# Kernel tuning notes

Measured on AMD Instinct MI355X. Metric: run time of the kernel, lower is better.

The kernel has to match this reference:

```python
import jax, jax.numpy as jnp
import numpy as np

HIDDEN = 128
N_H = 32
E = 262144


def setup_inputs() -> dict:
    key = jax.random.key(0)
    ks = jax.random.split(key, 10)
    s = lambda fan_in: 1.0 / np.sqrt(fan_in)
    return {
        "h_i": jax.random.normal(ks[0], (E, N_H), dtype=jnp.float32),
        "e_ij": jax.random.normal(ks[1], (E, 1), dtype=jnp.float32),
        # lin_A1: 1 -> HIDDEN
        "W_A1": jax.random.uniform(ks[2], (1, HIDDEN), jnp.float32, -s(1), s(1)),
        "b_A1": jnp.zeros((HIDDEN,), jnp.float32),
        # lin_A2: HIDDEN -> N_H*N_H
        "W_A2": jax.random.uniform(ks[3], (HIDDEN, N_H * N_H), jnp.float32, -s(HIDDEN), s(HIDDEN)),
        "b_A2": jnp.zeros((N_H * N_H,), jnp.float32),
        # lin_b1: 1 -> HIDDEN
        "W_b1": jax.random.uniform(ks[4], (1, HIDDEN), jnp.float32, -s(1), s(1)),
        "b_b1": jnp.zeros((HIDDEN,), jnp.float32),
        # lin_b2: HIDDEN -> N_H
        "W_b2": jax.random.uniform(ks[5], (HIDDEN, N_H), jnp.float32, -s(HIDDEN), s(HIDDEN)),
        "b_b2": jnp.zeros((N_H,), jnp.float32),
    }


def reference(h_i, e_ij, W_A1, b_A1, W_A2, b_A2, W_b1, b_b1, W_b2, b_b2):
    # Per-edge MLP producing an [N_H, N_H] matrix A from the scalar edge feature
    A = jax.nn.selu(e_ij @ W_A1 + b_A1)          # [E, HIDDEN]
    A = (A @ W_A2 + b_A2).reshape(-1, N_H, N_H)  # [E, N_H, N_H]
    # Per-edge MLP producing an [N_H] bias b
    b = jax.nn.selu(e_ij @ W_b1 + b_b1)          # [E, HIDDEN]
    b = b @ W_b2 + b_b2                          # [E, N_H]
    # Batched matvec: m_ij[e, i] = sum_j A[e, i, j] * h_i[e, j] + b[e, i]
    m_ij = jnp.einsum('eij,ej->ei', A, h_i) + b
    return m_ij
```

## Files before the change

kernel.cpp:

```cpp
#include <hip/hip_runtime.h>

#define NH      32
#define HID     128
#define E_TOT   262144
#define P_WT    4352
#define K_EXT   4256
#define CH_S    16
#define NCHUNK  8
#define LDSW_P  520

typedef float        f32x4 __attribute__((ext_vector_type(4)));
typedef short        s16x8 __attribute__((ext_vector_type(8)));
typedef unsigned int u32x4 __attribute__((ext_vector_type(4)));

static __device__ __forceinline__ short f2bf(float f) {
    __bf16 b = (__bf16)f;
    return __builtin_bit_cast(short, b);
}
static __device__ __forceinline__ float selu_f(float x) {
    const float kScale  = 1.0507009873554804934193349852946f;
    const float kAlphaS = 1.7580993408473768599402175208123f;
    float neg = kAlphaS * (__expf(x) - 1.0f);
    return x > 0.0f ? kScale * x : neg;
}

__global__ void wt_build(const float* __restrict__ W_A2, const float* __restrict__ b_A2,
                         const float* __restrict__ W_b2, unsigned short* __restrict__ WT) {
    int gid = blockIdx.x * 256 + threadIdx.x;
    if (gid >= 32 * K_EXT) return;
    int i = gid / K_EXT;
    int kap = gid - i * K_EXT;
    float v;
    if (kap < 4096) {
        int k = kap >> 5, j = kap & 31;
        v = W_A2[k * 1024 + i * 32 + j];
    } else if (kap < 4128) {
        int j = kap - 4096;
        v = b_A2[i * 32 + j];
    } else {
        int t = kap - 4128;
        v = W_b2[t * 32 + i];
    }
    WT[i * P_WT + kap] = (unsigned short)f2bf(v);
}

typedef const __attribute__((address_space(1))) unsigned int GU32;
typedef __attribute__((address_space(3))) unsigned int LU32;
static __device__ __forceinline__ void gload_lds16(const void* g, void* l) {
    __builtin_amdgcn_global_load_lds((GU32*)g, (LU32*)l, 16, 0, 0);
}

__global__ void __launch_bounds__(256, 3)
msg_main(const float* __restrict__ h_i, const float* __restrict__ e_ij,
         const float* __restrict__ W_A1, const float* __restrict__ b_A1,
         const float* __restrict__ W_b1, const float* __restrict__ b_b1,
         const float* __restrict__ b_b2,
         const unsigned short* __restrict__ WT,
         float* __restrict__ out)
{
    __shared__ unsigned short ldsW[32 * LDSW_P];
    __shared__ float ut[CH_S][256];
    __shared__ float cA1[HID], cBA1[HID], cB1a[HID], cB1b[HID], cb2[NH];

    const int tid  = threadIdx.x;
    const int lane = tid & 63;
    const int wid  = tid >> 6;
    const int lrow = lane & 15;
    const int g    = lane >> 4;
    const int e0   = blockIdx.x * 256 + wid * 64;
    const int wbase = wid * 64;

    if (tid < HID) {
        cA1[tid]  = W_A1[tid];
        cBA1[tid] = b_A1[tid];
        cB1a[tid] = W_b1[tid];
        cB1b[tid] = b_b1[tid];
    }
    if (tid < NH) cb2[tid] = b_b2[tid];

    const float ev_fill = e_ij[blockIdx.x * 256 + tid];

    s16x8 hb[4];
    float ev[4];
    #pragma unroll
    for (int ct = 0; ct < 4; ++ct) {
        int er = e0 + ct * 16 + lrow;
        const float* hp = h_i + er * 32 + g * 8;
        f32x4 h0 = *(const f32x4*)hp;
        f32x4 h1 = *(const f32x4*)(hp + 4);
        #pragma unroll
        for (int p = 0; p < 4; ++p) {
            hb[ct][p]     = f2bf(h0[p]);
            hb[ct][p + 4] = f2bf(h1[p]);
        }
        ev[ct] = e_ij[er];
    }

    f32x4 acc[4][2];
    #pragma unroll
    for (int ct = 0; ct < 4; ++ct)
        #pragma unroll
        for (int it = 0; it < 2; ++it)
            acc[ct][it] = (f32x4){0.f, 0.f, 0.f, 0.f};
    const f32x4 zf = (f32x4){0.f, 0.f, 0.f, 0.f};

    __syncthreads();

    for (int c = 0; c < NCHUNK; ++c) {
        const int kap0 = c * CH_S * 32;

        #pragma unroll
        for (int r = 0; r < 8; ++r) {
            int i = wid * 8 + r;
            const unsigned short* src = WT + i * P_WT + kap0 + lane * 8;
            gload_lds16(src, &ldsW[i * LDSW_P]);
        }

        #pragma unroll
        for (int sl = 0; sl < CH_S; ++sl) {
            int s = c * CH_S + sl;
            ut[sl][tid] = selu_f(fmaf(ev_fill, cA1[s], cBA1[s]));
        }
        __syncthreads();

        #pragma unroll
        for (int sl = 0; sl < CH_S; ++sl) {
            u32x4 r0 = *(const u32x4*)&ldsW[lrow        * LDSW_P + sl * 32 + g * 8];
            u32x4 r1 = *(const u32x4*)&ldsW[(lrow + 16) * LDSW_P + sl * 32 + g * 8];
            s16x8 A0 = __builtin_bit_cast(s16x8, r0);
            s16x8 A1 = __builtin_bit_cast(s16x8, r1);
            const float* urow = &ut[sl][wbase];
            #pragma unroll
            for (int ct = 0; ct < 4; ++ct) {
                float uv = urow[ct * 16 + lrow];
                f32x4 t0 = __builtin_amdgcn_mfma_f32_16x16x32_bf16(A0, hb[ct], zf, 0, 0, 0);
                f32x4 t1 = __builtin_amdgcn_mfma_f32_16x16x32_bf16(A1, hb[ct], zf, 0, 0, 0);
                f32x4 u4 = (f32x4){uv, uv, uv, uv};
                acc[ct][0] = __builtin_elementwise_fma(t0, u4, acc[ct][0]);
                acc[ct][1] = __builtin_elementwise_fma(t1, u4, acc[ct][1]);
            }
        }
        __syncthreads();
    }

    {
        int i   = tid >> 3;
        int seg = tid & 7;
        const unsigned short* src = WT + i * P_WT + 4096 + seg * 20;
        unsigned short* dst = ldsW + i * LDSW_P + seg * 20;
        #pragma unroll
        for (int q = 0; q < 20; ++q) dst[q] = src[q];
    }
    __syncthreads();

    {
        u32x4 r0 = *(const u32x4*)&ldsW[lrow        * LDSW_P + g * 8];
        u32x4 r1 = *(const u32x4*)&ldsW[(lrow + 16) * LDSW_P + g * 8];
        s16x8 A0 = __builtin_bit_cast(s16x8, r0);
        s16x8 A1 = __builtin_bit_cast(s16x8, r1);
        #pragma unroll
        for (int ct = 0; ct < 4; ++ct) {
            acc[ct][0] = __builtin_amdgcn_mfma_f32_16x16x32_bf16(A0, hb[ct], acc[ct][0], 0, 0, 0);
            acc[ct][1] = __builtin_amdgcn_mfma_f32_16x16x32_bf16(A1, hb[ct], acc[ct][1], 0, 0, 0);
        }
    }

    #pragma unroll
    for (int q = 0; q < 4; ++q) {
        int tb = q * 32 + g * 8;
        f32x4 wb0 = *(const f32x4*)&cB1a[tb];
        f32x4 wb1 = *(const f32x4*)&cB1a[tb + 4];
        f32x4 bb0 = *(const f32x4*)&cB1b[tb];
        f32x4 bb1 = *(const f32x4*)&cB1b[tb + 4];
        u32x4 r0 = *(const u32x4*)&ldsW[lrow        * LDSW_P + (1 + q) * 32 + g * 8];
        u32x4 r1 = *(const u32x4*)&ldsW[(lrow + 16) * LDSW_P + (1 + q) * 32 + g * 8];
        s16x8 A0 = __builtin_bit_cast(s16x8, r0);
        s16x8 A1 = __builtin_bit_cast(s16x8, r1);
        #pragma unroll
        for (int ct = 0; ct < 4; ++ct) {
            s16x8 B;
            #pragma unroll
            for (int p = 0; p < 4; ++p) {
                B[p]     = f2bf(selu_f(fmaf(ev[ct], wb0[p], bb0[p])));
                B[p + 4] = f2bf(selu_f(fmaf(ev[ct], wb1[p], bb1[p])));
            }
            acc[ct][0] = __builtin_amdgcn_mfma_f32_16x16x32_bf16(A0, B, acc[ct][0], 0, 0, 0);
            acc[ct][1] = __builtin_amdgcn_mfma_f32_16x16x32_bf16(A1, B, acc[ct][1], 0, 0, 0);
        }
    }

    #pragma unroll
    for (int it = 0; it < 2; ++it) {
        f32x4 b2v = *(const f32x4*)&cb2[it * 16 + g * 4];
        #pragma unroll
        for (int ct = 0; ct < 4; ++ct) {
            int edge = e0 + ct * 16 + lrow;
            f32x4 vo = acc[ct][it] + b2v;
            *(f32x4*)&out[edge * 32 + it * 16 + g * 4] = vo;
        }
    }
}

extern "C" void kernel_launch(void* const* d_in, const int* in_sizes, int n_in,
                              void* d_out, int out_size, void* d_ws, size_t ws_size,
                              hipStream_t stream) {
    const float* h_i  = (const float*)d_in[0];
    const float* e_ij = (const float*)d_in[1];
    const float* W_A1 = (const float*)d_in[2];
    const float* b_A1 = (const float*)d_in[3];
    const float* W_A2 = (const float*)d_in[4];
    const float* b_A2 = (const float*)d_in[5];
    const float* W_b1 = (const float*)d_in[6];
    const float* b_b1 = (const float*)d_in[7];
    const float* W_b2 = (const float*)d_in[8];
    const float* b_b2 = (const float*)d_in[9];

    unsigned short* WT = (unsigned short*)d_ws;

    wt_build<<<(32 * K_EXT + 255) / 256, 256, 0, stream>>>(W_A2, b_A2, W_b2, WT);
    msg_main<<<E_TOT / 256, 256, 0, stream>>>(h_i, e_ij, W_A1, b_A1, W_b1, b_b1,
                                              b_b2, WT, (float*)d_out);
}
```

Baseline: 101.0 us.

## Double-buffer weight chunks with swizzled LDS and split output tiles across waves

Weight chunks now stream through a double-buffered, XOR-swizzled LDS layout, so the next chunk's global-to-LDS load overlaps the current chunk's MFMA work. Each wave now handles one 16-row output tile for 128 edges instead of both tiles for 64 edges. The per-slice SELU activations move from a shared LDS table into registers and are broadcast with shuffles. This frees LDS to allow 4 blocks per SM, at the cost of more live registers per thread and shuffle overhead. The weight build now zero-fills the padded tail so the full chunk loads read defined data.

Result: slower. 125.4 us (+24.2%).

```diff
diff --git a/kernel.cpp b/kernel.cpp
--- a/kernel.cpp
+++ b/kernel.cpp
@@ -5,9 +5,8 @@
 #define E_TOT   262144
 #define P_WT    4352
 #define K_EXT   4256
-#define CH_S    16
-#define NCHUNK  8
-#define LDSW_P  520
+#define CH_S    8
+#define NCH     16
 
 typedef float        f32x4 __attribute__((ext_vector_type(4)));
 typedef short        s16x8 __attribute__((ext_vector_type(8)));
@@ -27,17 +26,17 @@
 __global__ void wt_build(const float* __restrict__ W_A2, const float* __restrict__ b_A2,
                          const float* __restrict__ W_b2, unsigned short* __restrict__ WT) {
     int gid = blockIdx.x * 256 + threadIdx.x;
-    if (gid >= 32 * K_EXT) return;
-    int i = gid / K_EXT;
-    int kap = gid - i * K_EXT;
-    float v;
+    if (gid >= 32 * P_WT) return;
+    int i = gid / P_WT;
+    int kap = gid - i * P_WT;
+    float v = 0.0f;
     if (kap < 4096) {
         int k = kap >> 5, j = kap & 31;
         v = W_A2[k * 1024 + i * 32 + j];
     } else if (kap < 4128) {
         int j = kap - 4096;
         v = b_A2[i * 32 + j];
-    } else {
+    } else if (kap < K_EXT) {
         int t = kap - 4128;
         v = W_b2[t * 32 + i];
     }
@@ -50,7 +49,7 @@
     __builtin_amdgcn_global_load_lds((GU32*)g, (LU32*)l, 16, 0, 0);
 }
 
-__global__ void __launch_bounds__(256, 3)
+__global__ void __launch_bounds__(256, 4)
 msg_main(const float* __restrict__ h_i, const float* __restrict__ e_ij,
          const float* __restrict__ W_A1, const float* __restrict__ b_A1,
          const float* __restrict__ W_b1, const float* __restrict__ b_b1,
@@ -58,17 +57,17 @@
          const unsigned short* __restrict__ WT,
          float* __restrict__ out)
 {
-    __shared__ unsigned short ldsW[32 * LDSW_P];
-    __shared__ float ut[CH_S][256];
+    __shared__ unsigned short ldsW[2][32][256];
     __shared__ float cA1[HID], cBA1[HID], cB1a[HID], cB1b[HID], cb2[NH];
 
-    const int tid  = threadIdx.x;
-    const int lane = tid & 63;
-    const int wid  = tid >> 6;
-    const int lrow = lane & 15;
-    const int g    = lane >> 4;
-    const int e0   = blockIdx.x * 256 + wid * 64;
-    const int wbase = wid * 64;
+    const int tid   = threadIdx.x;
+    const int lane  = tid & 63;
+    const int wid   = tid >> 6;
+    const int lrow  = lane & 15;
+    const int g     = lane >> 4;
+    const int itile = wid & 1;
+    const int eh    = wid >> 1;
+    const int we    = blockIdx.x * 256 + eh * 128;
 
     if (tid < HID) {
         cA1[tid]  = W_A1[tid];
@@ -78,13 +77,13 @@
     }
     if (tid < NH) cb2[tid] = b_b2[tid];
 
-    const float ev_fill = e_ij[blockIdx.x * 256 + tid];
-
-    s16x8 hb[4];
-    float ev[4];
-    #pragma unroll
-    for (int ct = 0; ct < 4; ++ct) {
-        int er = e0 + ct * 16 + lrow;
+    const float ev_lo = e_ij[we + lane];
+    const float ev_hi = e_ij[we + 64 + lane];
+
+    s16x8 hb[8];
+    #pragma unroll
+    for (int ct = 0; ct < 8; ++ct) {
+        int er = we + ct * 16 + lrow;
         const float* hp = h_i + er * 32 + g * 8;
         f32x4 h0 = *(const f32x4*)hp;
         f32x4 h1 = *(const f32x4*)(hp + 4);
@@ -93,111 +92,100 @@
             hb[ct][p]     = f2bf(h0[p]);
             hb[ct][p + 4] = f2bf(h1[p]);
         }
-        ev[ct] = e_ij[er];
-    }
-
-    f32x4 acc[4][2];
-    #pragma unroll
-    for (int ct = 0; ct < 4; ++ct)
-        #pragma unroll
-        for (int it = 0; it < 2; ++it)
-            acc[ct][it] = (f32x4){0.f, 0.f, 0.f, 0.f};
+    }
+
+    f32x4 acc[8];
+    #pragma unroll
+    for (int ct = 0; ct < 8; ++ct) acc[ct] = (f32x4){0.f, 0.f, 0.f, 0.f};
     const f32x4 zf = (f32x4){0.f, 0.f, 0.f, 0.f};
 
-    __syncthreads();
-
-    for (int c = 0; c < NCHUNK; ++c) {
-        const int kap0 = c * CH_S * 32;
-
-        #pragma unroll
-        for (int r = 0; r < 8; ++r) {
-            int i = wid * 8 + r;
-            const unsigned short* src = WT + i * P_WT + kap0 + lane * 8;
-            gload_lds16(src, &ldsW[i * LDSW_P]);
-        }
-
+    float u_lo[CH_S], u_hi[CH_S];
+
+    const char* rowbase = (const char*)&ldsW[0][0][0] + (itile * 16 + lrow) * 512;
+    const int   sR      = (lrow & 7) << 4;
+
+    auto stage = [&](int b, int c) {
+        #pragma unroll
+        for (int rp = 0; rp < 4; ++rp) {
+            int i0 = wid * 8 + rp * 2;
+            int R  = i0 + (lane >> 5);
+            int cb = (lane & 31) * 16;
+            int se = R * P_WT + c * 256 + (((cb) ^ ((R & 7) << 4)) >> 1);
+            gload_lds16(WT + se, &ldsW[b][i0][0]);
+        }
+    };
+    auto ufill = [&](int c) {
         #pragma unroll
         for (int sl = 0; sl < CH_S; ++sl) {
             int s = c * CH_S + sl;
-            ut[sl][tid] = selu_f(fmaf(ev_fill, cA1[s], cBA1[s]));
-        }
+            u_lo[sl] = selu_f(fmaf(ev_lo, cA1[s], cBA1[s]));
+            u_hi[sl] = selu_f(fmaf(ev_hi, cA1[s], cBA1[s]));
+        }
+    };
+
+    stage(0, 0);
+    ufill(0);
+    __syncthreads();
+
+    int buf = 0;
+    for (int c = 0; c < NCH; ++c) {
+        stage(buf ^ 1, c + 1);
+        #pragma unroll
+        for (int sl = 0; sl < CH_S; ++sl) {
+            u32x4 ra = *(const u32x4*)(rowbase + buf * 16384 + ((sl * 64 + g * 16) ^ sR));
+            s16x8 A  = __builtin_bit_cast(s16x8, ra);
+            #pragma unroll
+            for (int ct = 0; ct < 8; ++ct) {
+                float uv = __shfl(ct < 4 ? u_lo[sl] : u_hi[sl], (ct & 3) * 16 + lrow);
+                f32x4 t  = __builtin_amdgcn_mfma_f32_16x16x32_bf16(A, hb[ct], zf, 0, 0, 0);
+                f32x4 u4 = (f32x4){uv, uv, uv, uv};
+                acc[ct]  = __builtin_elementwise_fma(t, u4, acc[ct]);
+            }
+        }
+        if (c + 1 < NCH) ufill(c + 1);
         __syncthreads();
-
-        #pragma unroll
-        for (int sl = 0; sl < CH_S; ++sl) {
-            u32x4 r0 = *(const u32x4*)&ldsW[lrow        * LDSW_P + sl * 32 + g * 8];
-            u32x4 r1 = *(const u32x4*)&ldsW[(lrow + 16) * LDSW_P + sl * 32 + g * 8];
-            s16x8 A0 = __builtin_bit_cast(s16x8, r0);
-            s16x8 A1 = __builtin_bit_cast(s16x8, r1);
-            const float* urow = &ut[sl][wbase];
-            #pragma unroll
-            for (int ct = 0; ct < 4; ++ct) {
-                float uv = urow[ct * 16 + lrow];
-                f32x4 t0 = __builtin_amdgcn_mfma_f32_16x16x32_bf16(A0, hb[ct], zf, 0, 0, 0);
-                f32x4 t1 = __builtin_amdgcn_mfma_f32_16x16x32_bf16(A1, hb[ct], zf, 0, 0, 0);
-                f32x4 u4 = (f32x4){uv, uv, uv, uv};
-                acc[ct][0] = __builtin_elementwise_fma(t0, u4, acc[ct][0]);
-                acc[ct][1] = __builtin_elementwise_fma(t1, u4, acc[ct][1]);
-            }
-        }
-        __syncthreads();
+        buf ^= 1;
     }
 
     {
-        int i   = tid >> 3;
-        int seg = tid & 7;
-        const unsigned short* src = WT + i * P_WT + 4096 + seg * 20;
-        unsigned short* dst = ldsW + i * LDSW_P + seg * 20;
-        #pragma unroll
-        for (int q = 0; q < 20; ++q) dst[q] = src[q];
-    }
-    __syncthreads();
-
-    {
-        u32x4 r0 = *(const u32x4*)&ldsW[lrow        * LDSW_P + g * 8];
-        u32x4 r1 = *(const u32x4*)&ldsW[(lrow + 16) * LDSW_P + g * 8];
-        s16x8 A0 = __builtin_bit_cast(s16x8, r0);
-        s16x8 A1 = __builtin_bit_cast(s16x8, r1);
-        #pragma unroll
-        for (int ct = 0; ct < 4; ++ct) {
-            acc[ct][0] = __builtin_amdgcn_mfma_f32_16x16x32_bf16(A0, hb[ct], acc[ct][0], 0, 0, 0);
-            acc[ct][1] = __builtin_amdgcn_mfma_f32_16x16x32_bf16(A1, hb[ct], acc[ct][1], 0, 0, 0);
-        }
-    }
+        u32x4 ra = *(const u32x4*)(rowbase + buf * 16384 + ((g * 16) ^ sR));
+        s16x8 A  = __builtin_bit_cast(s16x8, ra);
+        #pragma unroll
+        for (int ct = 0; ct < 8; ++ct)
+            acc[ct] = __builtin_amdgcn_mfma_f32_16x16x32_bf16(A, hb[ct], acc[ct], 0, 0, 0);
+    }
+    float ev[8];
+    #pragma unroll
+    for (int ct = 0; ct < 8; ++ct)
+        ev[ct] = __shfl(ct < 4 ? ev_lo : ev_hi, (ct & 3) * 16 + lrow);
 
     #pragma unroll
     for (int q = 0; q < 4; ++q) {
+        u32x4 ra = *(const u32x4*)(rowbase + buf * 16384 + (((q + 1) * 64 + g * 16) ^ sR));
+        s16x8 A  = __builtin_bit_cast(s16x8, ra);
         int tb = q * 32 + g * 8;
         f32x4 wb0 = *(const f32x4*)&cB1a[tb];
         f32x4 wb1 = *(const f32x4*)&cB1a[tb + 4];
         f32x4 bb0 = *(const f32x4*)&cB1b[tb];
         f32x4 bb1 = *(const f32x4*)&cB1b[tb + 4];
-        u32x4 r0 = *(const u32x4*)&ldsW[lrow        * LDSW_P + (1 + q) * 32 + g * 8];
-        u32x4 r1 = *(const u32x4*)&ldsW[(lrow + 16) * LDSW_P + (1 + q) * 32 + g * 8];
-        s16x8 A0 = __builtin_bit_cast(s16x8, r0);
-        s16x8 A1 = __builtin_bit_cast(s16x8, r1);
-        #pragma unroll
-        for (int ct = 0; ct < 4; ++ct) {
+        #pragma unroll
+        for (int ct = 0; ct < 8; ++ct) {
             s16x8 B;
             #pragma unroll
             for (int p = 0; p < 4; ++p) {
                 B[p]     = f2bf(selu_f(fmaf(ev[ct], wb0[p], bb0[p])));
                 B[p + 4] = f2bf(selu_f(fmaf(ev[ct], wb1[p], bb1[p])));
             }
-            acc[ct][0] = __builtin_amdgcn_mfma_f32_16x16x32_bf16(A0, B, acc[ct][0], 0, 0, 0);
-            acc[ct][1] = __builtin_amdgcn_mfma_f32_16x16x32_bf16(A1, B, acc[ct][1], 0, 0, 0);
-        }
-    }
-
-    #pragma unroll
-    for (int it = 0; it < 2; ++it) {
-        f32x4 b2v = *(const f32x4*)&cb2[it * 16 + g * 4];
-        #pragma unroll
-        for (int ct = 0; ct < 4; ++ct) {
-            int edge = e0 + ct * 16 + lrow;
-            f32x4 vo = acc[ct][it] + b2v;
-            *(f32x4*)&out[edge * 32 + it * 16 + g * 4] = vo;
-        }
+            acc[ct] = __builtin_amdgcn_mfma_f32_16x16x32_bf16(A, B, acc[ct], 0, 0, 0);
+        }
+    }
+
+    f32x4 b2v = *(const f32x4*)&cb2[itile * 16 + g * 4];
+    #pragma unroll
+    for (int ct = 0; ct < 8; ++ct) {
+        int edge = we + ct * 16 + lrow;
+        f32x4 vo = acc[ct] + b2v;
+        *(f32x4*)&out[edge * 32 + itile * 16 + g * 4] = vo;
     }
 }
 
@@ -217,7 +205,7 @@
 
     unsigned short* WT = (unsigned short*)d_ws;
 
-    wt_build<<<(32 * K_EXT + 255) / 256, 256, 0, stream>>>(W_A2, b_A2, W_b2, WT);
+    wt_build<<<(32 * P_WT + 255) / 256, 256, 0, stream>>>(W_A2, b_A2, W_b2, WT);
     msg_main<<<E_TOT / 256, 256, 0, stream>>>(h_i, e_ij, W_A1, b_A1, W_b1, b_b1,
                                               b_b2, WT, (float*)d_out);
 }
```

## Double-buffer pre-swizzled weight chunks in LDS and shuffle SELU values across lanes

Applied to the files above, without the earlier changes.

Repacks the transformed weights into contiguous chunk tiles laid out in MFMA fragment order. The main loop can then double-buffer 16 chunks in LDS, loading chunk c+1 while chunk c is computed, with one barrier per chunk instead of two. The per-slot SELU activations now stay in registers and are broadcast with lane shuffles rather than staged through an LDS table. The bias and b-MLP weights move into a seventeenth chunk, which replaces the scalar copy loop. The costs are twice as many chunk iterations, extra shuffle instructions, and possible LDS bank conflicts from the unpadded 64-byte row stride.

New measurement: 109.8 us. 1.09x slower.

```diff
diff --git a/kernel.cpp b/kernel.cpp
--- a/kernel.cpp
+++ b/kernel.cpp
@@ -1,13 +1,11 @@
 #include <hip/hip_runtime.h>
 
-#define NH      32
-#define HID     128
-#define E_TOT   262144
-#define P_WT    4352
-#define K_EXT   4256
-#define CH_S    16
-#define NCHUNK  8
-#define LDSW_P  520
+#define NH       32
+#define HID      128
+#define E_TOT    262144
+#define CH_ELEM  8192
+#define NCH_MAIN 16
+#define NCH_ALL  17
 
 typedef float        f32x4 __attribute__((ext_vector_type(4)));
 typedef short        s16x8 __attribute__((ext_vector_type(8)));
@@ -27,21 +25,21 @@
 __global__ void wt_build(const float* __restrict__ W_A2, const float* __restrict__ b_A2,
                          const float* __restrict__ W_b2, unsigned short* __restrict__ WT) {
     int gid = blockIdx.x * 256 + threadIdx.x;
-    if (gid >= 32 * K_EXT) return;
-    int i = gid / K_EXT;
-    int kap = gid - i * K_EXT;
-    float v;
-    if (kap < 4096) {
-        int k = kap >> 5, j = kap & 31;
-        v = W_A2[k * 1024 + i * 32 + j];
-    } else if (kap < 4128) {
-        int j = kap - 4096;
-        v = b_A2[i * 32 + j];
-    } else {
-        int t = kap - 4128;
-        v = W_b2[t * 32 + i];
-    }
-    WT[i * P_WT + kap] = (unsigned short)f2bf(v);
+    if (gid >= NCH_ALL * CH_ELEM) return;
+    int c    = gid >> 13;
+    int r    = gid & 8191;
+    int sl   = r >> 10;
+    int it   = (r >> 9) & 1;
+    int lrow = (r >> 5) & 15;
+    int g    = (r >> 3) & 3;
+    int p    = r & 7;
+    int i    = it * 16 + lrow;
+    int kap  = c * 256 + sl * 32 + g * 8 + p;
+    float v = 0.0f;
+    if (kap < 4096)      v = W_A2[(kap >> 5) * 1024 + i * 32 + (kap & 31)];
+    else if (kap < 4128) v = b_A2[i * 32 + (kap - 4096)];
+    else if (kap < 4256) v = W_b2[(kap - 4128) * 32 + i];
+    WT[gid] = (unsigned short)f2bf(v);
 }
 
 typedef const __attribute__((address_space(1))) unsigned int GU32;
@@ -58,8 +56,7 @@
          const unsigned short* __restrict__ WT,
          float* __restrict__ out)
 {
-    __shared__ unsigned short ldsW[32 * LDSW_P];
-    __shared__ float ut[CH_S][256];
+    __shared__ unsigned short ldsW[2][CH_ELEM];
     __shared__ float cA1[HID], cBA1[HID], cB1a[HID], cB1b[HID], cb2[NH];
 
     const int tid  = threadIdx.x;
@@ -68,7 +65,6 @@
     const int lrow = lane & 15;
     const int g    = lane >> 4;
     const int e0   = blockIdx.x * 256 + wid * 64;
-    const int wbase = wid * 64;
 
     if (tid < HID) {
         cA1[tid]  = W_A1[tid];
@@ -78,10 +74,9 @@
     }
     if (tid < NH) cb2[tid] = b_b2[tid];
 
-    const float ev_fill = e_ij[blockIdx.x * 256 + tid];
+    const float ev_own = e_ij[e0 + lane];
 
     s16x8 hb[4];
-    float ev[4];
     #pragma unroll
     for (int ct = 0; ct < 4; ++ct) {
         int er = e0 + ct * 16 + lrow;
@@ -93,8 +88,11 @@
             hb[ct][p]     = f2bf(h0[p]);
             hb[ct][p + 4] = f2bf(h1[p]);
         }
-        ev[ct] = e_ij[er];
-    }
+    }
+
+    float ev_ct[4];
+    #pragma unroll
+    for (int ct = 0; ct < 4; ++ct) ev_ct[ct] = __shfl(ev_own, ct * 16 + lrow);
 
     f32x4 acc[4][2];
     #pragma unroll
@@ -104,35 +102,40 @@
             acc[ct][it] = (f32x4){0.f, 0.f, 0.f, 0.f};
     const f32x4 zf = (f32x4){0.f, 0.f, 0.f, 0.f};
 
+    float u_own[8];
+
+    auto stage = [&](int b, int c) {
+        #pragma unroll
+        for (int r = 0; r < 4; ++r) {
+            int eo = wid * 2048 + r * 512;
+            gload_lds16(WT + c * CH_ELEM + eo + lane * 8, &ldsW[b][eo]);
+        }
+    };
+    auto ufill = [&](int c) {
+        #pragma unroll
+        for (int sl = 0; sl < 8; ++sl) {
+            int s = c * 8 + sl;
+            u_own[sl] = selu_f(fmaf(ev_own, cA1[s], cBA1[s]));
+        }
+    };
+
     __syncthreads();
-
-    for (int c = 0; c < NCHUNK; ++c) {
-        const int kap0 = c * CH_S * 32;
-
-        #pragma unroll
-        for (int r = 0; r < 8; ++r) {
-            int i = wid * 8 + r;
-            const unsigned short* src = WT + i * P_WT + kap0 + lane * 8;
-            gload_lds16(src, &ldsW[i * LDSW_P]);
-        }
-
-        #pragma unroll
-        for (int sl = 0; sl < CH_S; ++sl) {
-            int s = c * CH_S + sl;
-            ut[sl][tid] = selu_f(fmaf(ev_fill, cA1[s], cBA1[s]));
-        }
-        __syncthreads();
-
-        #pragma unroll
-        for (int sl = 0; sl < CH_S; ++sl) {
-            u32x4 r0 = *(const u32x4*)&ldsW[lrow        * LDSW_P + sl * 32 + g * 8];
-            u32x4 r1 = *(const u32x4*)&ldsW[(lrow + 16) * LDSW_P + sl * 32 + g * 8];
+    stage(0, 0);
+    ufill(0);
+    __syncthreads();
+
+    int buf = 0;
+    for (int c = 0; c < NCH_MAIN; ++c) {
+        stage(buf ^ 1, c + 1);
+        #pragma unroll
+        for (int sl = 0; sl < 8; ++sl) {
+            u32x4 r0 = *(const u32x4*)&ldsW[buf][sl * 1024 +       lrow * 32 + g * 8];
+            u32x4 r1 = *(const u32x4*)&ldsW[buf][sl * 1024 + 512 + lrow * 32 + g * 8];
             s16x8 A0 = __builtin_bit_cast(s16x8, r0);
             s16x8 A1 = __builtin_bit_cast(s16x8, r1);
-            const float* urow = &ut[sl][wbase];
             #pragma unroll
             for (int ct = 0; ct < 4; ++ct) {
-                float uv = urow[ct * 16 + lrow];
+                float uv = __shfl(u_own[sl], ct * 16 + lrow);
                 f32x4 t0 = __builtin_amdgcn_mfma_f32_16x16x32_bf16(A0, hb[ct], zf, 0, 0, 0);
                 f32x4 t1 = __builtin_amdgcn_mfma_f32_16x16x32_bf16(A1, hb[ct], zf, 0, 0, 0);
                 f32x4 u4 = (f32x4){uv, uv, uv, uv};
@@ -140,22 +143,14 @@
                 acc[ct][1] = __builtin_elementwise_fma(t1, u4, acc[ct][1]);
             }
         }
+        if (c + 1 < NCH_MAIN) ufill(c + 1);
         __syncthreads();
+        buf ^= 1;
     }
 
     {
-        int i   = tid >> 3;
-        int seg = tid & 7;
-        const unsigned short* src = WT + i * P_WT + 4096 + seg * 20;
-        unsigned short* dst = ldsW + i * LDSW_P + seg * 20;
-        #pragma unroll
-        for (int q = 0; q < 20; ++q) dst[q] = src[q];
-    }
-    __syncthreads();
-
-    {
-        u32x4 r0 = *(const u32x4*)&ldsW[lrow        * LDSW_P + g * 8];
-        u32x4 r1 = *(const u32x4*)&ldsW[(lrow + 16) * LDSW_P + g * 8];
+        u32x4 r0 = *(const u32x4*)&ldsW[buf][      lrow * 32 + g * 8];
+        u32x4 r1 = *(const u32x4*)&ldsW[buf][512 + lrow * 32 + g * 8];
         s16x8 A0 = __builtin_bit_cast(s16x8, r0);
         s16x8 A1 = __builtin_bit_cast(s16x8, r1);
         #pragma unroll
@@ -164,25 +159,24 @@
             acc[ct][1] = __builtin_amdgcn_mfma_f32_16x16x32_bf16(A1, hb[ct], acc[ct][1], 0, 0, 0);
         }
     }
-
     #pragma unroll
     for (int q = 0; q < 4; ++q) {
+        u32x4 r0 = *(const u32x4*)&ldsW[buf][(q + 1) * 1024 +       lrow * 32 + g * 8];
+        u32x4 r1 = *(const u32x4*)&ldsW[buf][(q + 1) * 1024 + 512 + lrow * 32 + g * 8];
+        s16x8 A0 = __builtin_bit_cast(s16x8, r0);
+        s16x8 A1 = __builtin_bit_cast(s16x8, r1);
         int tb = q * 32 + g * 8;
         f32x4 wb0 = *(const f32x4*)&cB1a[tb];
         f32x4 wb1 = *(const f32x4*)&cB1a[tb + 4];
         f32x4 bb0 = *(const f32x4*)&cB1b[tb];
         f32x4 bb1 = *(const f32x4*)&cB1b[tb + 4];
-        u32x4 r0 = *(const u32x4*)&ldsW[lrow        * LDSW_P + (1 + q) * 32 + g * 8];
-        u32x4 r1 = *(const u32x4*)&ldsW[(lrow + 16) * LDSW_P + (1 + q) * 32 + g * 8];
-        s16x8 A0 = __builtin_bit_cast(s16x8, r0);
-        s16x8 A1 = __builtin_bit_cast(s16x8, r1);
         #pragma unroll
         for (int ct = 0; ct < 4; ++ct) {
             s16x8 B;
             #pragma unroll
             for (int p = 0; p < 4; ++p) {
-                B[p]     = f2bf(selu_f(fmaf(ev[ct], wb0[p], bb0[p])));
-                B[p + 4] = f2bf(selu_f(fmaf(ev[ct], wb1[p], bb1[p])));
+                B[p]     = f2bf(selu_f(fmaf(ev_ct[ct], wb0[p], bb0[p])));
+                B[p + 4] = f2bf(selu_f(fmaf(ev_ct[ct], wb1[p], bb1[p])));
             }
             acc[ct][0] = __builtin_amdgcn_mfma_f32_16x16x32_bf16(A0, B, acc[ct][0], 0, 0, 0);
             acc[ct][1] = __builtin_amdgcn_mfma_f32_16x16x32_bf16(A1, B, acc[ct][1], 0, 0, 0);
@@ -217,7 +211,7 @@
 
     unsigned short* WT = (unsigned short*)d_ws;
 
-    wt_build<<<(32 * K_EXT + 255) / 256, 256, 0, stream>>>(W_A2, b_A2, W_b2, WT);
+    wt_build<<<(NCH_ALL * CH_ELEM + 255) / 256, 256, 0, stream>>>(W_A2, b_A2, W_b2, WT);
     msg_main<<<E_TOT / 256, 256, 0, stream>>>(h_i, e_ij, W_A1, b_A1, W_b1, b_b1,
                                               b_b2, WT, (float*)d_out);
 }
```
